# Performance work log

Hardware: AMD Instinct MI355X
Metric: run time of the kernel (lower is better)

## Reference

```python
import jax, jax.numpy as jnp
import numpy as np

D_MODEL = 1024
NUM_HEADS = 16
HEAD_DIM = D_MODEL // NUM_HEADS  # 64
B, S = 4, 2048


def setup_inputs() -> dict:
    key = jax.random.key(0)
    ks = jax.random.split(key, 10)
    scale = 1.0 / np.sqrt(D_MODEL)
    x = jax.random.normal(ks[0], (B, S, D_MODEL), dtype=jnp.float32)
    # per-head projection weights stacked over the head axis (matches ModuleList of Linears)
    Wq = jax.random.normal(ks[1], (NUM_HEADS, D_MODEL, HEAD_DIM), dtype=jnp.float32) * scale
    bq = jax.random.normal(ks[2], (NUM_HEADS, HEAD_DIM), dtype=jnp.float32) * 0.01
    Wk = jax.random.normal(ks[3], (NUM_HEADS, D_MODEL, HEAD_DIM), dtype=jnp.float32) * scale
    bk = jax.random.normal(ks[4], (NUM_HEADS, HEAD_DIM), dtype=jnp.float32) * 0.01
    Wv = jax.random.normal(ks[5], (NUM_HEADS, D_MODEL, HEAD_DIM), dtype=jnp.float32) * scale
    bv = jax.random.normal(ks[6], (NUM_HEADS, HEAD_DIM), dtype=jnp.float32) * 0.01
    Wo = jax.random.normal(ks[7], (D_MODEL, D_MODEL), dtype=jnp.float32) * scale
    bo = jax.random.normal(ks[8], (D_MODEL,), dtype=jnp.float32) * 0.01
    return {"hidden_state": x, "Wq": Wq, "bq": bq, "Wk": Wk, "bk": bk,
            "Wv": Wv, "bv": bv, "Wo": Wo, "bo": bo}


def reference(hidden_state, Wq, bq, Wk, bk, Wv, bv, Wo, bo):
    # q,k,v: [B, H, S, E]
    q = jnp.einsum('bsd,hde->bhse', hidden_state, Wq) + bq[None, :, None, :]
    k = jnp.einsum('bsd,hde->bhse', hidden_state, Wk) + bk[None, :, None, :]
    v = jnp.einsum('bsd,hde->bhse', hidden_state, Wv) + bv[None, :, None, :]
    scores = jnp.einsum('bhse,bhte->bhst', q, k) / jnp.sqrt(jnp.asarray(HEAD_DIM, q.dtype))
    weights = jax.nn.softmax(scores, axis=-1)  # [B, H, S, S]
    attn = jnp.einsum('bhst,bhte->bhse', weights, v)  # [B, H, S, E]
    # concat heads along feature dim (head order preserved)
    attn = jnp.transpose(attn, (0, 2, 1, 3)).reshape(hidden_state.shape[0], hidden_state.shape[1], D_MODEL)
    return attn @ Wo + bo
```

## Files before the change

### kernel.cpp

```cpp
#include <hip/hip_runtime.h>

typedef __bf16 bf16x8 __attribute__((ext_vector_type(8)));
typedef float f32x4 __attribute__((ext_vector_type(4)));
typedef unsigned int u32x4 __attribute__((ext_vector_type(4)));
typedef unsigned int u32x2 __attribute__((ext_vector_type(2)));
typedef unsigned short u16x8 __attribute__((ext_vector_type(8)));

#define MFMA_BF16(a, b, c) __builtin_amdgcn_mfma_f32_16x16x32_bf16((a), (b), (c), 0, 0, 0)

#define QSCALE 0.18033688011112043f

__device__ __forceinline__ unsigned short f2bf(float f) {
    unsigned int u = __builtin_bit_cast(unsigned int, f);
    u += 0x7FFFu + ((u >> 16) & 1u);
    return (unsigned short)(u >> 16);
}

#if __has_builtin(__builtin_amdgcn_cvt_pk_bf16_f32)
typedef __bf16 bf16x2 __attribute__((ext_vector_type(2)));
__device__ __forceinline__ unsigned int pack_bf16(float a, float b) {
    return __builtin_bit_cast(unsigned int, __builtin_amdgcn_cvt_pk_bf16_f32(a, b));
}
#else
__device__ __forceinline__ unsigned int pack_bf16(float a, float b) {
    unsigned int ua = __builtin_bit_cast(unsigned int, a);
    unsigned int ub = __builtin_bit_cast(unsigned int, b);
    ua += 0x7FFFu + ((ua >> 16) & 1u);
    ub += 0x7FFFu + ((ub >> 16) & 1u);
    return __builtin_amdgcn_perm(ub, ua, 0x07060302);
}
#endif

#if __has_builtin(__builtin_amdgcn_exp2f)
__device__ __forceinline__ float fast_exp2(float x) { return __builtin_amdgcn_exp2f(x); }
#else
__device__ __forceinline__ float fast_exp2(float x) { return exp2f(x); }
#endif

__device__ __forceinline__ bf16x8 ldfrag(const unsigned short* p) {
    return __builtin_bit_cast(bf16x8, *(const u32x4*)p);
}

typedef const __attribute__((address_space(1))) void* gas_t;
typedef __attribute__((address_space(3))) void* las_t;
__device__ __forceinline__ void dma16(const unsigned short* g, unsigned short* l) {
    __builtin_amdgcn_global_load_lds((gas_t)(const void*)g, (las_t)(void*)l, 16, 0, 0);
}


__global__ void cvt_x_kernel(const float* __restrict__ in, unsigned short* __restrict__ out) {
    long long t = (long long)blockIdx.x * 256 + threadIdx.x;
    const f32x4* p = (const f32x4*)in + t * 2;
    f32x4 v0 = p[0], v1 = p[1];
    u16x8 o;
    o[0] = f2bf(v0[0]); o[1] = f2bf(v0[1]); o[2] = f2bf(v0[2]); o[3] = f2bf(v0[3]);
    o[4] = f2bf(v1[0]); o[5] = f2bf(v1[1]); o[6] = f2bf(v1[2]); o[7] = f2bf(v1[3]);
    *((u16x8*)out + t) = o;
}

__global__ void cvt_wqkvT_kernel(const float* __restrict__ Wq, const float* __restrict__ Wk,
                                 const float* __restrict__ Wv, unsigned short* __restrict__ WT) {
    int n = blockIdx.x * 256 + threadIdx.x;
    int d0 = blockIdx.y * 8;
    int proj = n >> 10, rem = n & 1023, h = rem >> 6, e = rem & 63;
    const float* W = (proj == 0) ? Wq : (proj == 1) ? Wk : Wv;
    const float* src = W + (size_t)h * 65536 + (size_t)d0 * 64 + e;
    u16x8 o;
#pragma unroll
    for (int j = 0; j < 8; j++) o[j] = f2bf(src[j * 64]);
    *(u16x8*)(WT + (size_t)n * 1024 + d0) = o;
}

__global__ void cvt_woT_kernel(const float* __restrict__ Wo, unsigned short* __restrict__ WoT) {
    int n = blockIdx.x * 256 + threadIdx.x;
    int d0 = blockIdx.y * 8;
    const float* src = Wo + (size_t)d0 * 1024 + n;
    u16x8 o;
#pragma unroll
    for (int j = 0; j < 8; j++) o[j] = f2bf(src[j * 1024]);
    *(u16x8*)(WoT + (size_t)n * 1024 + d0) = o;
}

__global__ void transpose_v_kernel(const unsigned short* __restrict__ V, unsigned short* __restrict__ VT) {
    __shared__ unsigned short tile[64 * 72];
    int bh = blockIdx.y, t0 = blockIdx.x * 64;
    int tid = threadIdx.x;
    int r = tid >> 2, cq = (tid & 3) * 16;
    const unsigned short* g = V + ((size_t)bh * 2048 + t0 + r) * 64 + cq;
    *(u32x4*)(tile + r * 72 + cq) = *(const u32x4*)g;
    *(u32x4*)(tile + r * 72 + cq + 8) = *(const u32x4*)(g + 8);
    __syncthreads();
    int e = tid >> 2, ts = (tid & 3) * 16;
    u16x8 o0, o1;
#pragma unroll
    for (int i = 0; i < 8; i++) o0[i] = tile[(ts + i) * 72 + e];
#pragma unroll
    for (int i = 0; i < 8; i++) o1[i] = tile[(ts + 8 + i) * 72 + e];
    unsigned short* dst = VT + ((size_t)bh * 64 + e) * 2048 + t0 + ts;
    *(u16x8*)dst = o0;
    *(u16x8*)(dst + 8) = o1;
}


__global__ __launch_bounds__(256) void gemm_qkv_kernel(
    const unsigned short* __restrict__ A, const unsigned short* __restrict__ BT,
    const float* __restrict__ bq, const float* __restrict__ bk, const float* __restrict__ bv,
    unsigned short* __restrict__ Qo, unsigned short* __restrict__ Ko, unsigned short* __restrict__ Vo) {
    __shared__ unsigned short As[128 * 32];
    __shared__ unsigned short Bs[128 * 32];
    const int tid = threadIdx.x;
    const int m0 = blockIdx.y * 128, n0 = blockIdx.x * 128;
    const int w = tid >> 6, lane = tid & 63, lr = lane & 15, quad = lane >> 4;
    const int wy = w >> 1, wx = w & 1;
    f32x4 acc[4][4];
#pragma unroll
    for (int i = 0; i < 4; i++)
#pragma unroll
        for (int j = 0; j < 4; j++) acc[i][j] = (f32x4){0.f, 0.f, 0.f, 0.f};
    const int drow = lane >> 2;
    const int dchunk = (lane & 3) ^ (drow & 3);
    const unsigned short* gA = A + (size_t)(m0 + w * 32 + drow) * 1024 + dchunk * 8;
    const unsigned short* gB = BT + (size_t)(n0 + w * 32 + drow) * 1024 + dchunk * 8;
    unsigned short* sA = As + (w * 32) * 32;
    unsigned short* sB = Bs + (w * 32) * 32;
    const int fcol = (quad ^ (lr & 3)) * 8;
    for (int k0 = 0; k0 < 1024; k0 += 32) {
        __syncthreads();
        dma16(gA + k0, sA);
        dma16(gA + k0 + 16 * 1024, sA + 16 * 32);
        dma16(gB + k0, sB);
        dma16(gB + k0 + 16 * 1024, sB + 16 * 32);
        __syncthreads();
        bf16x8 af[4], bfr[4];
#pragma unroll
        for (int i = 0; i < 4; i++) af[i] = ldfrag(As + (wy * 64 + i * 16 + lr) * 32 + fcol);
#pragma unroll
        for (int j = 0; j < 4; j++) bfr[j] = ldfrag(Bs + (wx * 64 + j * 16 + lr) * 32 + fcol);
#pragma unroll
        for (int i = 0; i < 4; i++)
#pragma unroll
            for (int j = 0; j < 4; j++) acc[i][j] = MFMA_BF16(af[i], bfr[j], acc[i][j]);
    }
#pragma unroll
    for (int j = 0; j < 4; j++) {
        int n = n0 + wx * 64 + j * 16 + lr;
        int proj = n >> 10, rem = n & 1023, h = rem >> 6, e = rem & 63;
        const float* bias = (proj == 0) ? bq : (proj == 1) ? bk : bv;
        unsigned short* dst = (proj == 0) ? Qo : (proj == 1) ? Ko : Vo;
        float bb = bias[rem];
        float scl = (proj == 0) ? QSCALE : 1.0f;
#pragma unroll
        for (int i = 0; i < 4; i++) {
#pragma unroll
            for (int r = 0; r < 4; r++) {
                int m = m0 + wy * 64 + i * 16 + quad * 4 + r;
                int batch = m >> 11, s = m & 2047;
                dst[(((size_t)batch * 16 + h) * 2048 + s) * 64 + e] = f2bf((acc[i][j][r] + bb) * scl);
            }
        }
    }
}

__global__ __launch_bounds__(256) void gemm_out_kernel(
    const unsigned short* __restrict__ A, const unsigned short* __restrict__ BT,
    const float* __restrict__ bo, float* __restrict__ out) {
    __shared__ unsigned short As[128 * 32];
    __shared__ unsigned short Bs[128 * 32];
    const int tid = threadIdx.x;
    const int m0 = blockIdx.y * 128, n0 = blockIdx.x * 128;
    const int w = tid >> 6, lane = tid & 63, lr = lane & 15, quad = lane >> 4;
    const int wy = w >> 1, wx = w & 1;
    f32x4 acc[4][4];
#pragma unroll
    for (int i = 0; i < 4; i++)
#pragma unroll
        for (int j = 0; j < 4; j++) acc[i][j] = (f32x4){0.f, 0.f, 0.f, 0.f};
    const int drow = lane >> 2;
    const int dchunk = (lane & 3) ^ (drow & 3);
    const unsigned short* gA = A + (size_t)(m0 + w * 32 + drow) * 1024 + dchunk * 8;
    const unsigned short* gB = BT + (size_t)(n0 + w * 32 + drow) * 1024 + dchunk * 8;
    unsigned short* sA = As + (w * 32) * 32;
    unsigned short* sB = Bs + (w * 32) * 32;
    const int fcol = (quad ^ (lr & 3)) * 8;
    for (int k0 = 0; k0 < 1024; k0 += 32) {
        __syncthreads();
        dma16(gA + k0, sA);
        dma16(gA + k0 + 16 * 1024, sA + 16 * 32);
        dma16(gB + k0, sB);
        dma16(gB + k0 + 16 * 1024, sB + 16 * 32);
        __syncthreads();
        bf16x8 af[4], bfr[4];
#pragma unroll
        for (int i = 0; i < 4; i++) af[i] = ldfrag(As + (wy * 64 + i * 16 + lr) * 32 + fcol);
#pragma unroll
        for (int j = 0; j < 4; j++) bfr[j] = ldfrag(Bs + (wx * 64 + j * 16 + lr) * 32 + fcol);
#pragma unroll
        for (int i = 0; i < 4; i++)
#pragma unroll
            for (int j = 0; j < 4; j++) acc[i][j] = MFMA_BF16(af[i], bfr[j], acc[i][j]);
    }
#pragma unroll
    for (int j = 0; j < 4; j++) {
        int n = n0 + wx * 64 + j * 16 + lr;
        float bb = bo[n];
#pragma unroll
        for (int i = 0; i < 4; i++) {
#pragma unroll
            for (int r = 0; r < 4; r++) {
                int m = m0 + wy * 64 + i * 16 + quad * 4 + r;
                out[(size_t)m * 1024 + n] = acc[i][j][r] + bb;
            }
        }
    }
}

#define ST 72
__global__ __launch_bounds__(256) void attn_fa_kernel(
    const unsigned short* __restrict__ Q, const unsigned short* __restrict__ K,
    const unsigned short* __restrict__ VT, unsigned short* __restrict__ Out) {
    __shared__ unsigned short Ks[64 * 64];
    __shared__ unsigned short Vs[64 * 64];
    __shared__ unsigned short Ps[128 * ST];
    const int bh = blockIdx.y;
    const int q0 = blockIdx.x * 128;
    const int tid = threadIdx.x;
    const int w = tid >> 6, lane = tid & 63, lr = lane & 15, quad = lane >> 4;
    const unsigned short* Qh = Q + (size_t)bh * 2048 * 64;
    const unsigned short* Kh = K + (size_t)bh * 2048 * 64;
    const unsigned short* Vh = VT + (size_t)bh * 64 * 2048;

    {
        int r = tid >> 1, c = (tid & 1) * 32;
        const unsigned short* g = Qh + (size_t)(q0 + r) * 64 + c;
        unsigned short* s = Ps + r * ST + c;
        *(u32x4*)s = *(const u32x4*)g;
        *(u32x4*)(s + 8) = *(const u32x4*)(g + 8);
        *(u32x4*)(s + 16) = *(const u32x4*)(g + 16);
        *(u32x4*)(s + 24) = *(const u32x4*)(g + 24);
    }
    __syncthreads();
    bf16x8 qb[2][2];
#pragma unroll
    for (int nt = 0; nt < 2; nt++)
#pragma unroll
        for (int kc = 0; kc < 2; kc++)
            qb[nt][kc] = ldfrag(Ps + (w * 32 + nt * 16 + lr) * ST + kc * 32 + quad * 8);

    f32x4 o[2][4];
#pragma unroll
    for (int i = 0; i < 2; i++)
#pragma unroll
        for (int j = 0; j < 4; j++) o[i][j] = (f32x4){0.f, 0.f, 0.f, 0.f};
    float lp[2] = {0.f, 0.f};

    const int drow = lane >> 3;
    const int dchunk = (lane & 7) ^ drow;
    const unsigned short* gK = Kh + (size_t)(w * 16 + drow) * 64 + dchunk * 8;
    const unsigned short* gV = Vh + (size_t)(w * 16 + drow) * 2048 + dchunk * 8;
    unsigned short* sK = Ks + (w * 16) * 64;
    unsigned short* sV = Vs + (w * 16) * 64;

    for (int t0 = 0; t0 < 2048; t0 += 64) {
        __syncthreads();
        dma16(gK + (size_t)t0 * 64, sK);
        dma16(gK + (size_t)t0 * 64 + 8 * 64, sK + 8 * 64);
        dma16(gV + t0, sV);
        dma16(gV + t0 + 8 * 2048, sV + 8 * 64);
        __syncthreads();

        f32x4 sc[4][2];
#pragma unroll
        for (int mt = 0; mt < 4; mt++) {
            sc[mt][0] = (f32x4){0.f, 0.f, 0.f, 0.f};
            sc[mt][1] = (f32x4){0.f, 0.f, 0.f, 0.f};
        }
#pragma unroll
        for (int kc = 0; kc < 2; kc++)
#pragma unroll
            for (int mt = 0; mt < 4; mt++) {
                bf16x8 ka = ldfrag(Ks + (mt * 16 + lr) * 64 + (((kc * 4 + quad) ^ (lr & 7)) * 8));
                sc[mt][0] = MFMA_BF16(ka, qb[0][kc], sc[mt][0]);
                sc[mt][1] = MFMA_BF16(ka, qb[1][kc], sc[mt][1]);
            }

#pragma unroll
        for (int nt = 0; nt < 2; nt++) {
            unsigned short* prow = Ps + (w * 32 + nt * 16 + lr) * ST + quad * 4;
#pragma unroll
            for (int mt = 0; mt < 4; mt++) {
                float p0 = fast_exp2(sc[mt][nt][0]);
                float p1 = fast_exp2(sc[mt][nt][1]);
                float p2 = fast_exp2(sc[mt][nt][2]);
                float p3 = fast_exp2(sc[mt][nt][3]);
                lp[nt] += (p0 + p1) + (p2 + p3);
                u32x2 pk;
                pk[0] = pack_bf16(p0, p1);
                pk[1] = pack_bf16(p2, p3);
                *(u32x2*)(prow + mt * 16) = pk;
            }
        }

#pragma unroll
        for (int kc = 0; kc < 2; kc++) {
            bf16x8 pa0 = ldfrag(Ps + (w * 32 + lr) * ST + kc * 32 + quad * 8);
            bf16x8 pa1 = ldfrag(Ps + (w * 32 + 16 + lr) * ST + kc * 32 + quad * 8);
#pragma unroll
            for (int et = 0; et < 4; et++) {
                bf16x8 vb = ldfrag(Vs + (et * 16 + lr) * 64 + (((kc * 4 + quad) ^ (lr & 7)) * 8));
                o[0][et] = MFMA_BF16(pa0, vb, o[0][et]);
                o[1][et] = MFMA_BF16(pa1, vb, o[1][et]);
            }
        }
    }

#pragma unroll
    for (int nt = 0; nt < 2; nt++) {
        float l = lp[nt];
        l += __shfl_xor(l, 16, 64);
        l += __shfl_xor(l, 32, 64);
        lp[nt] = l;
    }

    const int h = bh & 15, b = bh >> 4;
#pragma unroll
    for (int mt = 0; mt < 2; mt++) {
#pragma unroll
        for (int r = 0; r < 4; r++) {
            float l = __shfl(lp[mt], quad * 4 + r, 16);
            float inv = 1.0f / l;
            int s = q0 + w * 32 + mt * 16 + quad * 4 + r;
#pragma unroll
            for (int et = 0; et < 4; et++) {
                int col = h * 64 + et * 16 + lr;
                Out[((size_t)(b * 2048 + s)) * 1024 + col] = f2bf(o[mt][et][r] * inv);
            }
        }
    }
}


extern "C" void kernel_launch(void* const* d_in, const int* in_sizes, int n_in,
                              void* d_out, int out_size, void* d_ws, size_t ws_size,
                              hipStream_t stream) {
    const float* x  = (const float*)d_in[0];
    const float* Wq = (const float*)d_in[1];
    const float* bq = (const float*)d_in[2];
    const float* Wk = (const float*)d_in[3];
    const float* bk = (const float*)d_in[4];
    const float* Wv = (const float*)d_in[5];
    const float* bv = (const float*)d_in[6];
    const float* Wo = (const float*)d_in[7];
    const float* bo = (const float*)d_in[8];
    float* out = (float*)d_out;

    char* ws = (char*)d_ws;
    unsigned short* xb    = (unsigned short*)(ws);
    unsigned short* WqkvT = (unsigned short*)(ws + 16777216);
    unsigned short* WoT   = (unsigned short*)(ws + 23068672);
    unsigned short* Qb    = (unsigned short*)(ws + 25165824);
    unsigned short* Kb    = (unsigned short*)(ws + 41943040);
    unsigned short* Vb    = (unsigned short*)(ws + 58720256);
    unsigned short* VTb   = (unsigned short*)(ws + 75497472);
    unsigned short* attn  = xb;

    cvt_x_kernel<<<dim3(4096), dim3(256), 0, stream>>>(x, xb);
    cvt_wqkvT_kernel<<<dim3(12, 128), dim3(256), 0, stream>>>(Wq, Wk, Wv, WqkvT);
    cvt_woT_kernel<<<dim3(4, 128), dim3(256), 0, stream>>>(Wo, WoT);
    gemm_qkv_kernel<<<dim3(24, 64), dim3(256), 0, stream>>>(xb, WqkvT, bq, bk, bv, Qb, Kb, Vb);
    transpose_v_kernel<<<dim3(32, 64), dim3(256), 0, stream>>>(Vb, VTb);
    attn_fa_kernel<<<dim3(16, 64), dim3(256), 0, stream>>>(Qb, Kb, VTb, attn);
    gemm_out_kernel<<<dim3(8, 64), dim3(256), 0, stream>>>(attn, WoT, bo, out);
}
```

Baseline: 318.9 us.

## Double-buffer LDS loads in GEMMs and attention, fuse V transpose into QKV epilogue

Both GEMM kernels and the flash-attention kernel now use two LDS buffers. The next K-tile's global-to-LDS DMA is issued after the current fragments are read, so there is one barrier per iteration instead of two and loads overlap with MFMA work. The QKV GEMM epilogue writes V directly in transposed layout as packed 4-element stores, which removes the separate transpose kernel and its round trip through memory. In exchange, LDS use doubles and register pressure rises from preloading K/V fragments in attention, which may lower occupancy. The waitcnt(0) before each barrier also forces the prefetch to complete before use.

Result: faster. 296.3 us (-7.1%).

```diff
diff --git a/kernel.cpp b/kernel.cpp
--- a/kernel.cpp
+++ b/kernel.cpp
@@ -16,19 +16,23 @@
     return (unsigned short)(u >> 16);
 }
 
-#if __has_builtin(__builtin_amdgcn_cvt_pk_bf16_f32)
-typedef __bf16 bf16x2 __attribute__((ext_vector_type(2)));
-__device__ __forceinline__ unsigned int pack_bf16(float a, float b) {
-    return __builtin_bit_cast(unsigned int, __builtin_amdgcn_cvt_pk_bf16_f32(a, b));
-}
-#else
-__device__ __forceinline__ unsigned int pack_bf16(float a, float b) {
+__device__ __forceinline__ unsigned int pack_bf16_rne(float a, float b) {
     unsigned int ua = __builtin_bit_cast(unsigned int, a);
     unsigned int ub = __builtin_bit_cast(unsigned int, b);
     ua += 0x7FFFu + ((ua >> 16) & 1u);
     ub += 0x7FFFu + ((ub >> 16) & 1u);
     return __builtin_amdgcn_perm(ub, ua, 0x07060302);
 }
+
+#if __has_builtin(__builtin_amdgcn_cvt_pk_bf16_f32)
+typedef __bf16 bf16x2 __attribute__((ext_vector_type(2)));
+__device__ __forceinline__ unsigned int pack_bf16(float a, float b) {
+    return __builtin_bit_cast(unsigned int, __builtin_amdgcn_cvt_pk_bf16_f32(a, b));
+}
+#else
+__device__ __forceinline__ unsigned int pack_bf16(float a, float b) {
+    return pack_bf16_rne(a, b);
+}
 #endif
 
 #if __has_builtin(__builtin_amdgcn_exp2f)
@@ -45,6 +49,11 @@
 typedef __attribute__((address_space(3))) void* las_t;
 __device__ __forceinline__ void dma16(const unsigned short* g, unsigned short* l) {
     __builtin_amdgcn_global_load_lds((gas_t)(const void*)g, (las_t)(void*)l, 16, 0, 0);
+}
+
+__device__ __forceinline__ void pipeline_barrier() {
+    __builtin_amdgcn_s_waitcnt(0);
+    __syncthreads();
 }
 
 
@@ -81,33 +90,13 @@
     *(u16x8*)(WoT + (size_t)n * 1024 + d0) = o;
 }
 
-__global__ void transpose_v_kernel(const unsigned short* __restrict__ V, unsigned short* __restrict__ VT) {
-    __shared__ unsigned short tile[64 * 72];
-    int bh = blockIdx.y, t0 = blockIdx.x * 64;
-    int tid = threadIdx.x;
-    int r = tid >> 2, cq = (tid & 3) * 16;
-    const unsigned short* g = V + ((size_t)bh * 2048 + t0 + r) * 64 + cq;
-    *(u32x4*)(tile + r * 72 + cq) = *(const u32x4*)g;
-    *(u32x4*)(tile + r * 72 + cq + 8) = *(const u32x4*)(g + 8);
-    __syncthreads();
-    int e = tid >> 2, ts = (tid & 3) * 16;
-    u16x8 o0, o1;
-#pragma unroll
-    for (int i = 0; i < 8; i++) o0[i] = tile[(ts + i) * 72 + e];
-#pragma unroll
-    for (int i = 0; i < 8; i++) o1[i] = tile[(ts + 8 + i) * 72 + e];
-    unsigned short* dst = VT + ((size_t)bh * 64 + e) * 2048 + t0 + ts;
-    *(u16x8*)dst = o0;
-    *(u16x8*)(dst + 8) = o1;
-}
-
 
 __global__ __launch_bounds__(256) void gemm_qkv_kernel(
     const unsigned short* __restrict__ A, const unsigned short* __restrict__ BT,
     const float* __restrict__ bq, const float* __restrict__ bk, const float* __restrict__ bv,
-    unsigned short* __restrict__ Qo, unsigned short* __restrict__ Ko, unsigned short* __restrict__ Vo) {
-    __shared__ unsigned short As[128 * 32];
-    __shared__ unsigned short Bs[128 * 32];
+    unsigned short* __restrict__ Qo, unsigned short* __restrict__ Ko, unsigned short* __restrict__ VTo) {
+    __shared__ unsigned short As[2 * 128 * 32];
+    __shared__ unsigned short Bs[2 * 128 * 32];
     const int tid = threadIdx.x;
     const int m0 = blockIdx.y * 128, n0 = blockIdx.x * 128;
     const int w = tid >> 6, lane = tid & 63, lr = lane & 15, quad = lane >> 4;
@@ -121,21 +110,29 @@
     const int dchunk = (lane & 3) ^ (drow & 3);
     const unsigned short* gA = A + (size_t)(m0 + w * 32 + drow) * 1024 + dchunk * 8;
     const unsigned short* gB = BT + (size_t)(n0 + w * 32 + drow) * 1024 + dchunk * 8;
-    unsigned short* sA = As + (w * 32) * 32;
-    unsigned short* sB = Bs + (w * 32) * 32;
+    const int swav = (w * 32) * 32;
     const int fcol = (quad ^ (lr & 3)) * 8;
+    dma16(gA, As + swav);
+    dma16(gA + 16 * 1024, As + swav + 16 * 32);
+    dma16(gB, Bs + swav);
+    dma16(gB + 16 * 1024, Bs + swav + 16 * 32);
     for (int k0 = 0; k0 < 1024; k0 += 32) {
-        __syncthreads();
-        dma16(gA + k0, sA);
-        dma16(gA + k0 + 16 * 1024, sA + 16 * 32);
-        dma16(gB + k0, sB);
-        dma16(gB + k0 + 16 * 1024, sB + 16 * 32);
-        __syncthreads();
+        const int cur = (k0 >> 5) & 1;
+        const unsigned short* cA = As + cur * 4096;
+        const unsigned short* cB = Bs + cur * 4096;
+        pipeline_barrier();
         bf16x8 af[4], bfr[4];
 #pragma unroll
-        for (int i = 0; i < 4; i++) af[i] = ldfrag(As + (wy * 64 + i * 16 + lr) * 32 + fcol);
-#pragma unroll
-        for (int j = 0; j < 4; j++) bfr[j] = ldfrag(Bs + (wx * 64 + j * 16 + lr) * 32 + fcol);
+        for (int i = 0; i < 4; i++) af[i] = ldfrag(cA + (wy * 64 + i * 16 + lr) * 32 + fcol);
+#pragma unroll
+        for (int j = 0; j < 4; j++) bfr[j] = ldfrag(cB + (wx * 64 + j * 16 + lr) * 32 + fcol);
+        if (k0 + 32 < 1024) {
+            const int nb = (cur ^ 1) * 4096 + swav;
+            dma16(gA + k0 + 32, As + nb);
+            dma16(gA + k0 + 32 + 16 * 1024, As + nb + 16 * 32);
+            dma16(gB + k0 + 32, Bs + nb);
+            dma16(gB + k0 + 32 + 16 * 1024, Bs + nb + 16 * 32);
+        }
 #pragma unroll
         for (int i = 0; i < 4; i++)
 #pragma unroll
@@ -145,17 +142,30 @@
     for (int j = 0; j < 4; j++) {
         int n = n0 + wx * 64 + j * 16 + lr;
         int proj = n >> 10, rem = n & 1023, h = rem >> 6, e = rem & 63;
-        const float* bias = (proj == 0) ? bq : (proj == 1) ? bk : bv;
-        unsigned short* dst = (proj == 0) ? Qo : (proj == 1) ? Ko : Vo;
-        float bb = bias[rem];
-        float scl = (proj == 0) ? QSCALE : 1.0f;
-#pragma unroll
-        for (int i = 0; i < 4; i++) {
-#pragma unroll
-            for (int r = 0; r < 4; r++) {
-                int m = m0 + wy * 64 + i * 16 + quad * 4 + r;
+        if (proj == 2) {
+            float bb = bv[rem];
+#pragma unroll
+            for (int i = 0; i < 4; i++) {
+                int m = m0 + wy * 64 + i * 16 + quad * 4;
                 int batch = m >> 11, s = m & 2047;
-                dst[(((size_t)batch * 16 + h) * 2048 + s) * 64 + e] = f2bf((acc[i][j][r] + bb) * scl);
+                u32x2 pk;
+                pk[0] = pack_bf16_rne(acc[i][j][0] + bb, acc[i][j][1] + bb);
+                pk[1] = pack_bf16_rne(acc[i][j][2] + bb, acc[i][j][3] + bb);
+                *(u32x2*)(VTo + (((size_t)batch * 16 + h) * 64 + e) * 2048 + s) = pk;
+            }
+        } else {
+            const float* bias = (proj == 0) ? bq : bk;
+            unsigned short* dst = (proj == 0) ? Qo : Ko;
+            float bb = bias[rem];
+            float scl = (proj == 0) ? QSCALE : 1.0f;
+#pragma unroll
+            for (int i = 0; i < 4; i++) {
+#pragma unroll
+                for (int r = 0; r < 4; r++) {
+                    int m = m0 + wy * 64 + i * 16 + quad * 4 + r;
+                    int batch = m >> 11, s = m & 2047;
+                    dst[(((size_t)batch * 16 + h) * 2048 + s) * 64 + e] = f2bf((acc[i][j][r] + bb) * scl);
+                }
             }
         }
     }
@@ -164,8 +174,8 @@
 __global__ __launch_bounds__(256) void gemm_out_kernel(
     const unsigned short* __restrict__ A, const unsigned short* __restrict__ BT,
     const float* __restrict__ bo, float* __restrict__ out) {
-    __shared__ unsigned short As[128 * 32];
-    __shared__ unsigned short Bs[128 * 32];
+    __shared__ unsigned short As[2 * 128 * 32];
+    __shared__ unsigned short Bs[2 * 128 * 32];
     const int tid = threadIdx.x;
     const int m0 = blockIdx.y * 128, n0 = blockIdx.x * 128;
     const int w = tid >> 6, lane = tid & 63, lr = lane & 15, quad = lane >> 4;
@@ -179,21 +189,29 @@
     const int dchunk = (lane & 3) ^ (drow & 3);
     const unsigned short* gA = A + (size_t)(m0 + w * 32 + drow) * 1024 + dchunk * 8;
     const unsigned short* gB = BT + (size_t)(n0 + w * 32 + drow) * 1024 + dchunk * 8;
-    unsigned short* sA = As + (w * 32) * 32;
-    unsigned short* sB = Bs + (w * 32) * 32;
+    const int swav = (w * 32) * 32;
     const int fcol = (quad ^ (lr & 3)) * 8;
+    dma16(gA, As + swav);
+    dma16(gA + 16 * 1024, As + swav + 16 * 32);
+    dma16(gB, Bs + swav);
+    dma16(gB + 16 * 1024, Bs + swav + 16 * 32);
     for (int k0 = 0; k0 < 1024; k0 += 32) {
-        __syncthreads();
-        dma16(gA + k0, sA);
-        dma16(gA + k0 + 16 * 1024, sA + 16 * 32);
-        dma16(gB + k0, sB);
-        dma16(gB + k0 + 16 * 1024, sB + 16 * 32);
-        __syncthreads();
+        const int cur = (k0 >> 5) & 1;
+        const unsigned short* cA = As + cur * 4096;
+        const unsigned short* cB = Bs + cur * 4096;
+        pipeline_barrier();
         bf16x8 af[4], bfr[4];
 #pragma unroll
-        for (int i = 0; i < 4; i++) af[i] = ldfrag(As + (wy * 64 + i * 16 + lr) * 32 + fcol);
-#pragma unroll
-        for (int j = 0; j < 4; j++) bfr[j] = ldfrag(Bs + (wx * 64 + j * 16 + lr) * 32 + fcol);
+        for (int i = 0; i < 4; i++) af[i] = ldfrag(cA + (wy * 64 + i * 16 + lr) * 32 + fcol);
+#pragma unroll
+        for (int j = 0; j < 4; j++) bfr[j] = ldfrag(cB + (wx * 64 + j * 16 + lr) * 32 + fcol);
+        if (k0 + 32 < 1024) {
+            const int nb = (cur ^ 1) * 4096 + swav;
+            dma16(gA + k0 + 32, As + nb);
+            dma16(gA + k0 + 32 + 16 * 1024, As + nb + 16 * 32);
+            dma16(gB + k0 + 32, Bs + nb);
+            dma16(gB + k0 + 32 + 16 * 1024, Bs + nb + 16 * 32);
+        }
 #pragma unroll
         for (int i = 0; i < 4; i++)
 #pragma unroll
@@ -218,8 +236,8 @@
 __global__ __launch_bounds__(256) void attn_fa_kernel(
     const unsigned short* __restrict__ Q, const unsigned short* __restrict__ K,
     const unsigned short* __restrict__ VT, unsigned short* __restrict__ Out) {
-    __shared__ unsigned short Ks[64 * 64];
-    __shared__ unsigned short Vs[64 * 64];
+    __shared__ unsigned short Ks[2 * 64 * 64];
+    __shared__ unsigned short Vs[2 * 64 * 64];
     __shared__ unsigned short Ps[128 * ST];
     const int bh = blockIdx.y;
     const int q0 = blockIdx.x * 128;
@@ -229,6 +247,16 @@
     const unsigned short* Kh = K + (size_t)bh * 2048 * 64;
     const unsigned short* Vh = VT + (size_t)bh * 64 * 2048;
 
+    const int drow = lane >> 3;
+    const int dchunk = (lane & 7) ^ drow;
+    const unsigned short* gK = Kh + (size_t)(w * 16 + drow) * 64 + dchunk * 8;
+    const unsigned short* gV = Vh + (size_t)(w * 16 + drow) * 2048 + dchunk * 8;
+    const int swav = (w * 16) * 64;
+    dma16(gK, Ks + swav);
+    dma16(gK + 8 * 64, Ks + swav + 8 * 64);
+    dma16(gV, Vs + swav);
+    dma16(gV + 8 * 2048, Vs + swav + 8 * 64);
+
     {
         int r = tid >> 1, c = (tid & 1) * 32;
         const unsigned short* g = Qh + (size_t)(q0 + r) * 64 + c;
@@ -238,7 +266,6 @@
         *(u32x4*)(s + 16) = *(const u32x4*)(g + 16);
         *(u32x4*)(s + 24) = *(const u32x4*)(g + 24);
     }
-    __syncthreads();
     bf16x8 qb[2][2];
 #pragma unroll
     for (int nt = 0; nt < 2; nt++)
@@ -253,20 +280,27 @@
         for (int j = 0; j < 4; j++) o[i][j] = (f32x4){0.f, 0.f, 0.f, 0.f};
     float lp[2] = {0.f, 0.f};
 
-    const int drow = lane >> 3;
-    const int dchunk = (lane & 7) ^ drow;
-    const unsigned short* gK = Kh + (size_t)(w * 16 + drow) * 64 + dchunk * 8;
-    const unsigned short* gV = Vh + (size_t)(w * 16 + drow) * 2048 + dchunk * 8;
-    unsigned short* sK = Ks + (w * 16) * 64;
-    unsigned short* sV = Vs + (w * 16) * 64;
-
     for (int t0 = 0; t0 < 2048; t0 += 64) {
-        __syncthreads();
-        dma16(gK + (size_t)t0 * 64, sK);
-        dma16(gK + (size_t)t0 * 64 + 8 * 64, sK + 8 * 64);
-        dma16(gV + t0, sV);
-        dma16(gV + t0 + 8 * 2048, sV + 8 * 64);
-        __syncthreads();
+        const int cur = (t0 >> 6) & 1;
+        const unsigned short* cK = Ks + cur * 4096;
+        const unsigned short* cV = Vs + cur * 4096;
+        pipeline_barrier();
+        bf16x8 ka[2][4], vb[2][4];
+#pragma unroll
+        for (int kc = 0; kc < 2; kc++)
+#pragma unroll
+            for (int mt = 0; mt < 4; mt++) {
+                int fc = ((kc * 4 + quad) ^ (lr & 7)) * 8;
+                ka[kc][mt] = ldfrag(cK + (mt * 16 + lr) * 64 + fc);
+                vb[kc][mt] = ldfrag(cV + (mt * 16 + lr) * 64 + fc);
+            }
+        if (t0 + 64 < 2048) {
+            const int nb = (cur ^ 1) * 4096 + swav;
+            dma16(gK + (size_t)(t0 + 64) * 64, Ks + nb);
+            dma16(gK + (size_t)(t0 + 64) * 64 + 8 * 64, Ks + nb + 8 * 64);
+            dma16(gV + t0 + 64, Vs + nb);
+            dma16(gV + t0 + 64 + 8 * 2048, Vs + nb + 8 * 64);
+        }
 
         f32x4 sc[4][2];
 #pragma unroll
@@ -278,9 +312,8 @@
         for (int kc = 0; kc < 2; kc++)
 #pragma unroll
             for (int mt = 0; mt < 4; mt++) {
-                bf16x8 ka = ldfrag(Ks + (mt * 16 + lr) * 64 + (((kc * 4 + quad) ^ (lr & 7)) * 8));
-                sc[mt][0] = MFMA_BF16(ka, qb[0][kc], sc[mt][0]);
-                sc[mt][1] = MFMA_BF16(ka, qb[1][kc], sc[mt][1]);
+                sc[mt][0] = MFMA_BF16(ka[kc][mt], qb[0][kc], sc[mt][0]);
+                sc[mt][1] = MFMA_BF16(ka[kc][mt], qb[1][kc], sc[mt][1]);
             }
 
 #pragma unroll
@@ -306,9 +339,8 @@
             bf16x8 pa1 = ldfrag(Ps + (w * 32 + 16 + lr) * ST + kc * 32 + quad * 8);
 #pragma unroll
             for (int et = 0; et < 4; et++) {
-                bf16x8 vb = ldfrag(Vs + (et * 16 + lr) * 64 + (((kc * 4 + quad) ^ (lr & 7)) * 8));
-                o[0][et] = MFMA_BF16(pa0, vb, o[0][et]);
-                o[1][et] = MFMA_BF16(pa1, vb, o[1][et]);
+                o[0][et] = MFMA_BF16(pa0, vb[kc][et], o[0][et]);
+                o[1][et] = MFMA_BF16(pa1, vb[kc][et], o[1][et]);
             }
         }
     }
@@ -359,15 +391,13 @@
     unsigned short* WoT   = (unsigned short*)(ws + 23068672);
     unsigned short* Qb    = (unsigned short*)(ws + 25165824);
     unsigned short* Kb    = (unsigned short*)(ws + 41943040);
-    unsigned short* Vb    = (unsigned short*)(ws + 58720256);
-    unsigned short* VTb   = (unsigned short*)(ws + 75497472);
+    unsigned short* VTb   = (unsigned short*)(ws + 58720256);
     unsigned short* attn  = xb;
 
     cvt_x_kernel<<<dim3(4096), dim3(256), 0, stream>>>(x, xb);
     cvt_wqkvT_kernel<<<dim3(12, 128), dim3(256), 0, stream>>>(Wq, Wk, Wv, WqkvT);
     cvt_woT_kernel<<<dim3(4, 128), dim3(256), 0, stream>>>(Wo, WoT);
-    gemm_qkv_kernel<<<dim3(24, 64), dim3(256), 0, stream>>>(xb, WqkvT, bq, bk, bv, Qb, Kb, Vb);
-    transpose_v_kernel<<<dim3(32, 64), dim3(256), 0, stream>>>(Vb, VTb);
+    gemm_qkv_kernel<<<dim3(24, 64), dim3(256), 0, stream>>>(xb, WqkvT, bq, bk, bv, Qb, Kb, VTb);
     attn_fa_kernel<<<dim3(16, 64), dim3(256), 0, stream>>>(Qb, Kb, VTb, attn);
     gemm_out_kernel<<<dim3(8, 64), dim3(256), 0, stream>>>(attn, WoT, bo, out);
 }
```
